# Performance work log

Hardware: AMD Instinct MI355X
Metric: run time of the kernel (lower is better)

The kernel has to match this reference:

```python
import jax, jax.numpy as jnp
import numpy as np

B, T, I, H, O = 128, 512, 64, 512, 1


def setup_inputs() -> dict:
    key = jax.random.key(0)
    ks = jax.random.split(key, 7)
    s = 1.0 / np.sqrt(H)  # torch default init scale
    return {
        "x": jax.random.normal(ks[0], (B, T, I), dtype=jnp.float32),
        "W_ih": jax.random.uniform(ks[1], (4 * H, I), jnp.float32, -s, s),
        "W_hh": jax.random.uniform(ks[2], (4 * H, H), jnp.float32, -s, s),
        "b_ih": jax.random.uniform(ks[3], (4 * H,), jnp.float32, -s, s),
        "b_hh": jax.random.uniform(ks[4], (4 * H,), jnp.float32, -s, s),
        "W_ho": jax.random.uniform(ks[5], (O, H), jnp.float32, -s, s),
        "b_ho": jax.random.uniform(ks[6], (O,), jnp.float32, -s, s),
    }


def reference(x, W_ih, W_hh, b_ih, b_hh, W_ho, b_ho):
    # Precompute input projections for all timesteps: [T, B, 4H]
    xg = jnp.einsum("bti,gi->tbg", x, W_ih) + b_ih + b_hh

    def step(carry, xg_t):
        h, c = carry
        gates = xg_t + h @ W_hh.T  # [B, 4H]
        i, f, g, o = jnp.split(gates, 4, axis=-1)  # torch LSTMCell gate order
        c = jax.nn.sigmoid(f) * c + jax.nn.sigmoid(i) * jnp.tanh(g)
        h = jax.nn.sigmoid(o) * jnp.tanh(c)
        return (h, c), h

    h0 = jnp.zeros((x.shape[0], W_hh.shape[1]), dtype=x.dtype)
    _, hs = jax.lax.scan(step, (h0, h0), xg)  # hs: [T, B, H]
    out = jnp.einsum("tbh,oh->bto", hs, W_ho) + b_ho  # [B, T, O]
    return out.squeeze(2)  # [B, T] since O == 1
```

## Files before the change

### kernel.cpp

```cpp
#include <hip/hip_runtime.h>


#define B_ 128
#define T_ 512
#define I_ 64
#define H_ 512

typedef __attribute__((ext_vector_type(8))) short short8;
typedef __attribute__((ext_vector_type(4))) float f32x4;
typedef __attribute__((ext_vector_type(4))) unsigned u32x4;

__device__ inline unsigned f2bf_u(float f) {
  union { float f; unsigned u; } v; v.f = f;
  return (v.u + 0x7fffu + ((v.u >> 16) & 1u)) >> 16;
}
__device__ inline float bf2f(unsigned s) {
  union { unsigned u; float f; } v; v.u = s << 16; return v.f;
}
__device__ inline float sigm(float x) { return 1.0f / (1.0f + __expf(-x)); }
__device__ inline float tanh_(float x) { return 1.0f - 2.0f / (1.0f + __expf(2.0f * x)); }

#define WAITV(N)                                        \
  asm volatile("s_waitcnt vmcnt(" #N ")" ::: "memory"); \
  __builtin_amdgcn_sched_barrier(0)

#define HLOADQ(dst, base, OFF)                                            \
  asm volatile("global_load_dwordx4 %0, %1, off offset:" #OFF " sc0 sc1"  \
               : "=v"(dst) : "v"(base))

#define XLOADQ(dst, base, OFF)                                            \
  asm volatile("global_load_dwordx4 %0, %1, off offset:" #OFF             \
               : "=v"(dst) : "v"(base))

#define HSTORED2(base, v64)                                               \
  asm volatile("global_store_dwordx2 %0, %1, off sc0 sc1"                 \
               :: "v"(base), "v"(v64) : "memory")

__global__ __launch_bounds__(256, 1) void lstm_kernel(
    const float* __restrict__ x,
    const float* __restrict__ Wih,
    const float* __restrict__ Whh,
    const float* __restrict__ bih,
    const float* __restrict__ bhh,
    const float* __restrict__ Who,
    float* __restrict__ part,
    unsigned short* __restrict__ hbuf,
    unsigned* __restrict__ flags)
{
  const int bid = blockIdx.x;
  const int jg = bid >> 3;
  const int bg = bid & 7;
  const int tid = threadIdx.x;
  const int w = tid >> 6;
  const int l = tid & 63;
  const int l16 = l & 15;
  const int lk = l >> 4;
  const int b = bg * 16 + l16;

  short8 a_hh[4][16], a_ih[4][2];
  float bias[4][4], who[4];
#pragma unroll
  for (int m = 0; m < 4; ++m) {
    const int rowA = w * 64 + m * 16 + l16;
    const int grow = (rowA & 3) * 512 + jg * 64 + (rowA >> 2);
#pragma unroll
    for (int kt = 0; kt < 16; ++kt) {
      const float* p = Whh + (size_t)grow * H_ + kt * 32 + lk * 8;
      short8 s;
#pragma unroll
      for (int e = 0; e < 8; ++e) s[e] = (short)f2bf_u(p[e]);
      a_hh[m][kt] = s;
    }
#pragma unroll
    for (int kt = 0; kt < 2; ++kt) {
      const float* p = Wih + (size_t)grow * I_ + kt * 32 + lk * 8;
      short8 s;
#pragma unroll
      for (int e = 0; e < 8; ++e) s[e] = (short)f2bf_u(p[e]);
      a_ih[m][kt] = s;
    }
    const int jm = jg * 64 + w * 16 + m * 4 + lk;
#pragma unroll
    for (int g = 0; g < 4; ++g) bias[m][g] = bih[g * 512 + jm] + bhh[g * 512 + jm];
    who[m] = Who[jm];
  }

  __shared__ unsigned short hlds[2][2][16][512];
#define HOFS(pl, bb, kt) (((((pl) * 16 + (bb)) * 512) + (kt) * 32 + lk * 8) ^ (((bb) & 7) << 3))

  unsigned short* const hb0 = hbuf;
  unsigned short* const hb1 = hbuf + 2 * B_ * H_;
  unsigned* const fbase = flags + (size_t)bg * 32;
  unsigned* const myflag = fbase + (jg * 4 + w);
  const float* const xrow = x + (size_t)b * (T_ * I_);

  float c[4] = {0.f, 0.f, 0.f, 0.f};
  f32x4 xf0, xf1, xf2, xf3;
  {
    const float* xb = xrow + lk * 8;
    XLOADQ(xf0, xb, 0);   XLOADQ(xf1, xb, 16);
    XLOADQ(xf2, xb, 128); XLOADQ(xf3, xb, 144);
    WAITV(0);
  }

  for (int t = 0; t < T_; ++t) {
    const int pr = t & 1;
    const unsigned short* hp = pr ? hb1 : hb0;
    unsigned short* hn       = pr ? hb0 : hb1;
    unsigned short* const hldsF = &hlds[pr][0][0][0];

    WAITV(4);

    f32x4 acc[4][2];
#pragma unroll
    for (int m = 0; m < 4; ++m) {
      acc[m][0] = (f32x4){0.f, 0.f, 0.f, 0.f};
      acc[m][1] = (f32x4){0.f, 0.f, 0.f, 0.f};
    }

#pragma unroll
    for (int kt = 0; kt < 2; ++kt) {
      f32x4 va = kt ? xf2 : xf0;
      f32x4 vb = kt ? xf3 : xf1;
      float v[8] = {va[0], va[1], va[2], va[3], vb[0], vb[1], vb[2], vb[3]};
      short8 xhi, xlo;
#pragma unroll
      for (int e = 0; e < 8; ++e) {
        unsigned hb = f2bf_u(v[e]);
        xhi[e] = (short)hb;
        xlo[e] = (short)f2bf_u(v[e] - bf2f(hb));
      }
#pragma unroll
      for (int m = 0; m < 4; ++m) {
        acc[m][0] = __builtin_amdgcn_mfma_f32_16x16x32_bf16(a_ih[m][kt], xhi, acc[m][0], 0, 0, 0);
        acc[m][1] = __builtin_amdgcn_mfma_f32_16x16x32_bf16(a_ih[m][kt], xlo, acc[m][1], 0, 0, 0);
      }
    }

    if (t > 0) {
      {
        const unsigned* fp = fbase + (l & 31);
        for (;;) {
          unsigned f = __hip_atomic_load(fp, __ATOMIC_RELAXED, __HIP_MEMORY_SCOPE_AGENT);
          if (__all(f >= (unsigned)t)) break;
        }
      }
      __builtin_amdgcn_fence(__ATOMIC_ACQUIRE, "workgroup");
      __builtin_amdgcn_sched_barrier(0);

      u32x4 qh[4], ql[4];
      const unsigned short* phh = hp + (size_t)b * H_ + w * 128 + lk * 8;
      const unsigned short* pll = phh + (size_t)(B_ * H_);
      HLOADQ(qh[0], phh, 0);   HLOADQ(qh[1], phh, 64);
      HLOADQ(qh[2], phh, 128); HLOADQ(qh[3], phh, 192);
      HLOADQ(ql[0], pll, 0);   HLOADQ(ql[1], pll, 64);
      HLOADQ(ql[2], pll, 128); HLOADQ(ql[3], pll, 192);
      {
        const int tn = (t + 1 < T_) ? t + 1 : t;
        const float* xb = xrow + tn * I_ + lk * 8;
        XLOADQ(xf0, xb, 0);   XLOADQ(xf1, xb, 16);
        XLOADQ(xf2, xb, 128); XLOADQ(xf3, xb, 144);
      }
      WAITV(4);

      const unsigned tlo = (unsigned)(t & 3);
      const unsigned thi = (unsigned)((t >> 2) & 3);
      for (;;) {
        unsigned bad = 0;
#pragma unroll
        for (int i = 0; i < 4; ++i) {
          bad |= (qh[i].x ^ tlo) | (qh[i].z ^ thi)
               | (ql[i].x ^ tlo) | (ql[i].z ^ thi);
        }
        bad &= 3u;
        if (__all(bad == 0)) break;
        HLOADQ(qh[0], phh, 0);   HLOADQ(qh[1], phh, 64);
        HLOADQ(qh[2], phh, 128); HLOADQ(qh[3], phh, 192);
        HLOADQ(ql[0], pll, 0);   HLOADQ(ql[1], pll, 64);
        HLOADQ(ql[2], pll, 128); HLOADQ(ql[3], pll, 192);
        WAITV(0);
      }
      __builtin_amdgcn_sched_barrier(0);

#pragma unroll
      for (int i = 0; i < 4; ++i) {
        *(u32x4*)&hldsF[HOFS(0, l16, 4 * w + i)] = qh[i];
        *(u32x4*)&hldsF[HOFS(1, l16, 4 * w + i)] = ql[i];
      }
      __syncthreads();

#pragma unroll
      for (int kt = 0; kt < 16; ++kt) {
        short8 fh = *(const short8*)&hldsF[HOFS(0, l16, kt)];
        short8 fl = *(const short8*)&hldsF[HOFS(1, l16, kt)];
#pragma unroll
        for (int m = 0; m < 4; ++m) {
          acc[m][0] = __builtin_amdgcn_mfma_f32_16x16x32_bf16(a_hh[m][kt], fh, acc[m][0], 0, 0, 0);
          acc[m][1] = __builtin_amdgcn_mfma_f32_16x16x32_bf16(a_hh[m][kt], fl, acc[m][1], 0, 0, 0);
        }
      }
    } else {
      const float* xb = xrow + I_ + lk * 8;
      XLOADQ(xf0, xb, 0);   XLOADQ(xf1, xb, 16);
      XLOADQ(xf2, xb, 128); XLOADQ(xf3, xb, 144);
    }

    const unsigned tgp = (unsigned)((t + 1) & 15);
    float p = 0.f;
    unsigned wd[4];
#pragma unroll
    for (int m = 0; m < 4; ++m) {
      float gi = sigm(acc[m][0].x + acc[m][1].x + bias[m][0]);
      float gf = sigm(acc[m][0].y + acc[m][1].y + bias[m][1]);
      float gg = tanh_(acc[m][0].z + acc[m][1].z + bias[m][2]);
      float go = sigm(acc[m][0].w + acc[m][1].w + bias[m][3]);
      c[m] = gf * c[m] + gi * gg;
      float hv = go * tanh_(c[m]);
      p += hv * who[m];
      unsigned tb = (m & 1) ? (tgp >> 2) : (tgp & 3u);
      unsigned hb = f2bf_u(hv);
      if (lk == 0) hb = (hb & ~3u) | tb;
      unsigned lo = f2bf_u(hv - bf2f(hb));
      if (lk == 0) lo = (lo & ~3u) | tb;
      wd[m] = hb | (lo << 16);
    }

    {
      unsigned r0[4], r1[4];
#pragma unroll
      for (int m = 0; m < 4; ++m) r0[m] = __shfl_xor(wd[m], 16);
#pragma unroll
      for (int m = 0; m < 4; ++m) if ((m ^ lk) & 1) wd[m] = r0[m ^ 1];
#pragma unroll
      for (int m = 0; m < 4; ++m) r1[m] = __shfl_xor(wd[m], 32);
#pragma unroll
      for (int m = 0; m < 4; ++m) if ((m ^ lk) & 2) wd[m] = r1[m ^ 2];
    }

    {
      unsigned hi01 = (wd[0] & 0xffffu) | (wd[1] << 16);
      unsigned hi23 = (wd[2] & 0xffffu) | (wd[3] << 16);
      unsigned lo01 = (wd[0] >> 16) | (wd[1] & 0xffff0000u);
      unsigned lo23 = (wd[2] >> 16) | (wd[3] & 0xffff0000u);
      unsigned long long hiq = (unsigned long long)hi01 | ((unsigned long long)hi23 << 32);
      unsigned long long loq = (unsigned long long)lo01 | ((unsigned long long)lo23 << 32);
      unsigned short* ph = hn + (size_t)b * H_ + jg * 64 + w * 16 + lk * 4;
      HSTORED2(ph, hiq);
      HSTORED2(ph + B_ * H_, loq);
    }
    if (l == 0)
      __hip_atomic_store(myflag, (unsigned)(t + 1),
                         __ATOMIC_RELAXED, __HIP_MEMORY_SCOPE_AGENT);

    p += __shfl_xor(p, 16);
    p += __shfl_xor(p, 32);
    if (l < 16) atomicAdd(part + ((size_t)jg * B_ + b) * T_ + t, p);
  }
#undef HOFS
}

__global__ __launch_bounds__(256) void reduce_out(const float* __restrict__ part,
                                                  const float* __restrict__ b_ho,
                                                  float* __restrict__ out) {
  int i = blockIdx.x * blockDim.x + threadIdx.x;
  if (i < B_ * T_) {
    float s = b_ho[0];
#pragma unroll
    for (int g = 0; g < 8; ++g) s += part[(size_t)g * B_ * T_ + i];
    out[i] = s;
  }
}

extern "C" void kernel_launch(void* const* d_in, const int* in_sizes, int n_in,
                              void* d_out, int out_size, void* d_ws, size_t ws_size,
                              hipStream_t stream) {
  (void)in_sizes; (void)n_in; (void)out_size; (void)ws_size;
  const float* x   = (const float*)d_in[0];
  const float* Wih = (const float*)d_in[1];
  const float* Whh = (const float*)d_in[2];
  const float* bih = (const float*)d_in[3];
  const float* bhh = (const float*)d_in[4];
  const float* Who = (const float*)d_in[5];
  const float* bho = (const float*)d_in[6];
  float* out = (float*)d_out;

  unsigned short* hbuf = (unsigned short*)d_ws;
  const size_t hbytes = (size_t)2 * 2 * B_ * H_ * sizeof(unsigned short);
  float* part = (float*)((char*)d_ws + hbytes);
  const size_t pbytes = (size_t)8 * B_ * T_ * sizeof(float);
  unsigned* flags = (unsigned*)((char*)d_ws + hbytes + pbytes);

  hipMemsetAsync((char*)d_ws + hbytes, 0, pbytes + 8 * 32 * sizeof(unsigned), stream);

  lstm_kernel<<<dim3(64), dim3(256), 0, stream>>>(x, Wih, Whh, bih, bhh, Who,
                                                  part, hbuf, flags);
  reduce_out<<<(B_ * T_ + 255) / 256, 256, 0, stream>>>(part, bho, out);
}
```

Before: 2.692 ms.

## Speculatively issue h loads before flag poll and replace atomics with plain partial stores

The h-state loads for the next step are now issued before the MFMA input projection and the flag spin, so their latency overlaps the wait; the per-element tag check still guards against stale data. The x prefetch is moved after validation. The flag store now waits for outstanding stores (vmcnt 0) before publishing. When the workspace is large enough, per-wave partial outputs are written with plain stores into a 32-slice buffer instead of atomicAdd, removing the memset of partials and atomic traffic, at the cost of a wider reduction kernel.

Measured after the change: 3.071 ms. 1.14x slower.

```diff
diff --git a/kernel.cpp b/kernel.cpp
--- a/kernel.cpp
+++ b/kernel.cpp
@@ -36,6 +36,7 @@
   asm volatile("global_store_dwordx2 %0, %1, off sc0 sc1"                 \
                :: "v"(base), "v"(v64) : "memory")
 
+template <int PLAIN>
 __global__ __launch_bounds__(256, 1) void lstm_kernel(
     const float* __restrict__ x,
     const float* __restrict__ Wih,
@@ -109,7 +110,15 @@
     unsigned short* hn       = pr ? hb0 : hb1;
     unsigned short* const hldsF = &hlds[pr][0][0][0];
 
-    WAITV(4);
+    u32x4 qh[4], ql[4];
+    const unsigned short* phh = hp + (size_t)b * H_ + w * 128 + lk * 8;
+    const unsigned short* pll = phh + (size_t)(B_ * H_);
+    if (t > 0) {
+      HLOADQ(qh[0], phh, 0);   HLOADQ(qh[1], phh, 64);
+      HLOADQ(qh[2], phh, 128); HLOADQ(qh[3], phh, 192);
+      HLOADQ(ql[0], pll, 0);   HLOADQ(ql[1], pll, 64);
+      HLOADQ(ql[2], pll, 128); HLOADQ(ql[3], pll, 192);
+    }
 
     f32x4 acc[4][2];
 #pragma unroll
@@ -147,21 +156,7 @@
       }
       __builtin_amdgcn_fence(__ATOMIC_ACQUIRE, "workgroup");
       __builtin_amdgcn_sched_barrier(0);
-
-      u32x4 qh[4], ql[4];
-      const unsigned short* phh = hp + (size_t)b * H_ + w * 128 + lk * 8;
-      const unsigned short* pll = phh + (size_t)(B_ * H_);
-      HLOADQ(qh[0], phh, 0);   HLOADQ(qh[1], phh, 64);
-      HLOADQ(qh[2], phh, 128); HLOADQ(qh[3], phh, 192);
-      HLOADQ(ql[0], pll, 0);   HLOADQ(ql[1], pll, 64);
-      HLOADQ(ql[2], pll, 128); HLOADQ(ql[3], pll, 192);
-      {
-        const int tn = (t + 1 < T_) ? t + 1 : t;
-        const float* xb = xrow + tn * I_ + lk * 8;
-        XLOADQ(xf0, xb, 0);   XLOADQ(xf1, xb, 16);
-        XLOADQ(xf2, xb, 128); XLOADQ(xf3, xb, 144);
-      }
-      WAITV(4);
+      WAITV(0);
 
       const unsigned tlo = (unsigned)(t & 3);
       const unsigned thi = (unsigned)((t >> 2) & 3);
@@ -181,6 +176,13 @@
         WAITV(0);
       }
       __builtin_amdgcn_sched_barrier(0);
+
+      {
+        const int tn = (t + 1 < T_) ? t + 1 : t;
+        const float* xb = xrow + tn * I_ + lk * 8;
+        XLOADQ(xf0, xb, 0);   XLOADQ(xf1, xb, 16);
+        XLOADQ(xf2, xb, 128); XLOADQ(xf3, xb, 144);
+      }
 
 #pragma unroll
       for (int i = 0; i < 4; ++i) {
@@ -248,17 +250,26 @@
       HSTORED2(ph, hiq);
       HSTORED2(ph + B_ * H_, loq);
     }
+
+    p += __shfl_xor(p, 16);
+    p += __shfl_xor(p, 32);
+
+    WAITV(0);
     if (l == 0)
       __hip_atomic_store(myflag, (unsigned)(t + 1),
                          __ATOMIC_RELAXED, __HIP_MEMORY_SCOPE_AGENT);
 
-    p += __shfl_xor(p, 16);
-    p += __shfl_xor(p, 32);
-    if (l < 16) atomicAdd(part + ((size_t)jg * B_ + b) * T_ + t, p);
+    if (l < 16) {
+      if constexpr (PLAIN != 0)
+        part[(((size_t)jg * 4 + w) * B_ + b) * T_ + t] = p;
+      else
+        atomicAdd(part + ((size_t)jg * B_ + b) * T_ + t, p);
+    }
   }
 #undef HOFS
 }
 
+template <int NP>
 __global__ __launch_bounds__(256) void reduce_out(const float* __restrict__ part,
                                                   const float* __restrict__ b_ho,
                                                   float* __restrict__ out) {
@@ -266,7 +277,7 @@
   if (i < B_ * T_) {
     float s = b_ho[0];
 #pragma unroll
-    for (int g = 0; g < 8; ++g) s += part[(size_t)g * B_ * T_ + i];
+    for (int g = 0; g < NP; ++g) s += part[(size_t)g * B_ * T_ + i];
     out[i] = s;
   }
 }
@@ -274,7 +285,7 @@
 extern "C" void kernel_launch(void* const* d_in, const int* in_sizes, int n_in,
                               void* d_out, int out_size, void* d_ws, size_t ws_size,
                               hipStream_t stream) {
-  (void)in_sizes; (void)n_in; (void)out_size; (void)ws_size;
+  (void)in_sizes; (void)n_in; (void)out_size;
   const float* x   = (const float*)d_in[0];
   const float* Wih = (const float*)d_in[1];
   const float* Whh = (const float*)d_in[2];
@@ -287,12 +298,22 @@
   unsigned short* hbuf = (unsigned short*)d_ws;
   const size_t hbytes = (size_t)2 * 2 * B_ * H_ * sizeof(unsigned short);
   float* part = (float*)((char*)d_ws + hbytes);
-  const size_t pbytes = (size_t)8 * B_ * T_ * sizeof(float);
-  unsigned* flags = (unsigned*)((char*)d_ws + hbytes + pbytes);
-
-  hipMemsetAsync((char*)d_ws + hbytes, 0, pbytes + 8 * 32 * sizeof(unsigned), stream);
-
-  lstm_kernel<<<dim3(64), dim3(256), 0, stream>>>(x, Wih, Whh, bih, bhh, Who,
-                                                  part, hbuf, flags);
-  reduce_out<<<(B_ * T_ + 255) / 256, 256, 0, stream>>>(part, bho, out);
-}
+
+  const size_t pbytes32 = (size_t)32 * B_ * T_ * sizeof(float);
+  const size_t pbytes8  = (size_t)8 * B_ * T_ * sizeof(float);
+  const size_t fbytes   = 8 * 32 * sizeof(unsigned);
+
+  if (ws_size >= hbytes + pbytes32 + fbytes) {
+    unsigned* flags = (unsigned*)((char*)d_ws + hbytes + pbytes32);
+    hipMemsetAsync(flags, 0, fbytes, stream);
+    lstm_kernel<1><<<dim3(64), dim3(256), 0, stream>>>(x, Wih, Whh, bih, bhh,
+                                                       Who, part, hbuf, flags);
+    reduce_out<32><<<(B_ * T_ + 255) / 256, 256, 0, stream>>>(part, bho, out);
+  } else {
+    unsigned* flags = (unsigned*)((char*)d_ws + hbytes + pbytes8);
+    hipMemsetAsync(part, 0, pbytes8 + fbytes, stream);
+    lstm_kernel<0><<<dim3(64), dim3(256), 0, stream>>>(x, Wih, Whh, bih, bhh,
+                                                       Who, part, hbuf, flags);
+    reduce_out<8><<<(B_ * T_ + 255) / 256, 256, 0, stream>>>(part, bho, out);
+  }
+}
```
